# Kernel tuning notes

Measured on AMD Instinct MI355X. Metric: run time of the kernel, lower is better.

Reference implementation:

```python
import math
import jax, jax.numpy as jnp
import numpy as np

C1, D, NUM_HEADS, K_CH = 150, 32, 4, 10
GLOBAL_TOPK_RATIO = 0.08


def _pos2d(h, w, dim):
    d2 = dim // 2
    div = jnp.exp(jnp.arange(0, d2, 2, dtype=jnp.float32) * (-(math.log(10000.0) / d2)))
    def axis_pe(n):
        ang = jnp.arange(n, dtype=jnp.float32)[:, None] * div[None, :]
        pe = jnp.zeros((n, d2), dtype=jnp.float32)
        pe = pe.at[:, 0::2].set(jnp.sin(ang))
        pe = pe.at[:, 1::2].set(jnp.cos(ang))
        return pe
    pe_y = axis_pe(h)  # [h, d2]
    pe_x = axis_pe(w)  # [w, d2]
    return jnp.concatenate([
        jnp.broadcast_to(pe_y[:, None, :], (h, w, d2)),
        jnp.broadcast_to(pe_x[None, :, :], (h, w, d2)),
    ], axis=-1)  # [h, w, dim]


def setup_inputs() -> dict:
    key = jax.random.key(0)
    ks = jax.random.split(key, 7)
    B = 1024
    return {
        "x": jax.random.uniform(ks[0], (B, 1, 28, 28), dtype=jnp.float32),
        "conv1_w": jax.random.normal(ks[1], (C1, 1, 9, 9), dtype=jnp.float32) * 0.05,
        "channel_embed": jax.random.normal(ks[2], (C1, D), dtype=jnp.float32) * 0.02,
        "in_proj_w": jax.random.normal(ks[3], (3 * D, D), dtype=jnp.float32) * (1.0 / math.sqrt(D)),
        "in_proj_b": jnp.zeros((3 * D,), dtype=jnp.float32),
        "out_proj_w": jax.random.normal(ks[4], (D, D), dtype=jnp.float32) * (1.0 / math.sqrt(D)),
        "out_proj_b": jnp.zeros((D,), dtype=jnp.float32),
    }


def reference(x, conv1_w, channel_embed, in_proj_w, in_proj_b, out_proj_w, out_proj_b):
    # conv1 + relu: [B,1,28,28] -> [B,150,14,14]
    A = jax.nn.relu(jax.lax.conv_general_dilated(
        x, conv1_w, window_strides=(2, 2), padding=((4, 4), (4, 4)),
        dimension_numbers=("NCHW", "OIHW", "NCHW")))
    B, C, H, W = A.shape
    total = C * H * W
    k_global = max(1, int(math.ceil(GLOBAL_TOPK_RATIO * total)))
    A_flat = A.reshape(B, -1)
    # global kthvalue threshold: k_global-th largest per sample
    thresh = jax.lax.top_k(A_flat, k_global)[0][:, -1:]
    A_global = (A_flat * (A_flat >= thresh)).reshape(B, C, H, W)
    # per-location channel top-k + scatter
    v = jnp.transpose(A_global, (0, 2, 3, 1))  # [B,H,W,C]
    topv, topi = jax.lax.top_k(v, K_CH)        # [B,H,W,k]
    N = B * H * W
    logits = jnp.zeros((N, C), v.dtype).at[
        jnp.arange(N)[:, None], topi.reshape(N, K_CH)
    ].set(topv.reshape(N, K_CH)).reshape(v.shape)
    # normalize by per-sample global max (guard zero)
    flat_logits = logits.reshape(B, -1)
    gmax = jnp.max(flat_logits, axis=1, keepdims=True)
    normed = jnp.where(gmax == 0, 0.0, flat_logits / jnp.where(gmax == 0, 1.0, gmax))
    sparse_weights = normed.reshape(logits.shape)  # [B,H,W,C]
    # channel embedding + 2D sinusoidal PE
    loc_emb = jnp.einsum("bhwc,cd->bhwd", sparse_weights, channel_embed)
    loc_emb = loc_emb + _pos2d(H, W, D)[None]
    seq = loc_emb.reshape(B, H * W, D)
    # 1-layer MHA (self-attention, batch_first)
    qkv = seq @ in_proj_w.T + in_proj_b  # [B,S,3D]
    q, k, vv = jnp.split(qkv, 3, axis=-1)
    hd = D // NUM_HEADS
    def heads(t):
        return jnp.transpose(t.reshape(B, H * W, NUM_HEADS, hd), (0, 2, 1, 3))
    q, k, vv = heads(q), heads(k), heads(vv)
    attn = jax.nn.softmax(jnp.einsum("bnsd,bntd->bnst", q, k) / math.sqrt(hd), axis=-1)
    ctx = jnp.einsum("bnst,bntd->bnsd", attn, vv)
    ctx = jnp.transpose(ctx, (0, 2, 1, 3)).reshape(B, H * W, D)
    attn_out = ctx @ out_proj_w.T + out_proj_b  # [B, 196, 32]
    return attn_out
```

## Files before the change

kernel.cpp:

```cpp
#include <hip/hip_runtime.h>
#include <math.h>

#define NC1 150
#define HW 196
#define NB 1024
#define DD 32
#define NHD 4
#define HDIM 8
#define KG 2352
#define KCH 10
#define CAP 48
#define CVS 49
#define CES 36
#define KVS 20

typedef float v2f __attribute__((ext_vector_type(2)));

__device__ __forceinline__ float dot32v(const v2f* __restrict__ xr2,
                                        const float* __restrict__ wr, float bias) {
  const float4* w4 = (const float4*)wr;
  v2f s0 = {bias, 0.f};
  v2f s1 = {0.f, 0.f};
#pragma unroll
  for (int e = 0; e < 8; ++e) {
    float4 w = w4[e];
    v2f wlo = {w.x, w.y}, whi = {w.z, w.w};
    s0 = __builtin_elementwise_fma(xr2[2 * e], wlo, s0);
    s1 = __builtin_elementwise_fma(xr2[2 * e + 1], whi, s1);
  }
  v2f s = s0 + s1;
  return s.x + s.y;
}

#define UNI_F 17552
#define XT_OFF 0
#define WT_OFF 8232
#define CV_OFF 0
#define CC_OFF 9604
#define CNT_OFF 11956
#define CE_OFF 12152

__global__ void prep2_kernel(const float* __restrict__ cw, float* __restrict__ wtg,
                             float* __restrict__ pos) {
  int i = blockIdx.x * 256 + threadIdx.x;
  if (i < HW * DD) {
    int s = i >> 5, d = i & 31;
    int h = s / 14, w = s % 14;
    int p = (d < 16) ? h : w;
    int dd = (d < 16) ? d : d - 16;
    int j = dd >> 1;
    float dv = expf(-(logf(10000.0f) / 16.0f) * (float)(2 * j));
    float ang = (float)p * dv;
    pos[i] = (dd & 1) ? cosf(ang) : sinf(ang);
    return;
  }
  int j = i - HW * DD;
  if (j < 84 * 152) {
    int k = j / 152, c = j - k * 152;
    wtg[j] = (k < 81 && c < NC1) ? cw[c * 81 + k] : 0.f;
  }
}

__global__ __launch_bounds__(1024, 8) void fused_kernel(const float* __restrict__ x,
                                                        const float* __restrict__ wtg,
                                                        const float* __restrict__ CE,
                                                        const float* __restrict__ pos,
                                                        float* __restrict__ seqo) {
  __shared__ alignas(16) float uni[UNI_F];
  __shared__ alignas(16) float xs[784];
  __shared__ unsigned hist[2048];
  __shared__ unsigned wsum[4];
  __shared__ unsigned s_prefix, s_krem, s_max;

  int b = blockIdx.x, tid = threadIdx.x;
  int lane = tid & 63, wid = tid >> 6;

  if (tid < 196) ((float4*)xs)[tid] = ((const float4*)(x + (size_t)b * 784))[tid];
  if (tid == 0) { s_prefix = 0u; s_krem = KG; s_max = 0u; }
  __syncthreads();

  int cg = tid / 49;
  int g  = tid - cg * 49;
  bool act = (tid < 931);
  float acc[4][8];
#pragma unroll
  for (int i = 0; i < 4; ++i)
#pragma unroll
    for (int j = 0; j < 8; ++j) acc[i][j] = 0.f;

  float* XT = uni + XT_OFF;
  float* WT = uni + WT_OFF;

  for (int kb = 0; kb < 84; kb += 42) {
    for (int i = tid; i < 42 * 196; i += 1024) {
      int kk = i / 196, s = i - kk * 196;
      int k = kb + kk;
      float v = 0.f;
      if (k < 81) {
        int ki = k / 9, kj = k - ki * 9;
        int h = s / 14, w = s - h * 14;
        int r = 2 * h - 4 + ki, c = 2 * w - 4 + kj;
        if (r >= 0 && r < 28 && c >= 0 && c < 28) v = xs[r * 28 + c];
      }
      XT[i] = v;
    }
    for (int i = tid; i < (42 * 152) / 4; i += 1024)
      ((float4*)WT)[i] = ((const float4*)(wtg + kb * 152))[i];
    __syncthreads();
    if (act) {
      const float* xtp = XT + 4 * g;
      const float* wtp = WT + 8 * cg;
#pragma unroll 7
      for (int kk = 0; kk < 42; ++kk) {
        float4 xv = *(const float4*)(xtp + kk * 196);
        float4 w0 = *(const float4*)(wtp + kk * 152);
        float4 w1 = *(const float4*)(wtp + kk * 152 + 4);
        float xa[4] = {xv.x, xv.y, xv.z, xv.w};
        float wa[8] = {w0.x, w0.y, w0.z, w0.w, w1.x, w1.y, w1.z, w1.w};
#pragma unroll
        for (int i = 0; i < 4; ++i)
#pragma unroll
          for (int j = 0; j < 8; ++j) acc[i][j] += xa[i] * wa[j];
      }
    }
    __syncthreads();
  }

#pragma unroll
  for (int i = 0; i < 4; ++i)
#pragma unroll
    for (int j = 0; j < 8; ++j) acc[i][j] = fmaxf(acc[i][j], 0.f);

  for (int pass = 0; pass < 3; ++pass) {
    hist[tid] = 0u; hist[tid + 1024] = 0u;
    __syncthreads();
    int shift = (pass == 0) ? 21 : (pass == 1 ? 10 : 0);
    int bits = (pass == 2) ? 10 : 11;
    unsigned mask = (1u << bits) - 1u;
    unsigned pfx = s_prefix;
    unsigned krem = s_krem;
    int hishift = shift + bits;
    if (pass == 0) {
      unsigned mymax = 0u;
#pragma unroll
      for (int i = 0; i < 4; ++i)
#pragma unroll
        for (int j = 0; j < 8; ++j) {
          unsigned u = __float_as_uint(acc[i][j]);
          mymax = max(mymax, u);
          if (u) atomicAdd(&hist[u >> 21], 1u);
        }
#pragma unroll
      for (int st = 32; st >= 1; st >>= 1)
        mymax = max(mymax, (unsigned)__shfl_xor((int)mymax, st));
      if (lane == 0) atomicMax(&s_max, mymax);
    } else {
#pragma unroll
      for (int i = 0; i < 4; ++i)
#pragma unroll
        for (int j = 0; j < 8; ++j) {
          unsigned u = __float_as_uint(acc[i][j]);
          if (u && (u >> hishift) == pfx) atomicAdd(&hist[(u >> shift) & mask], 1u);
        }
    }
    __syncthreads();
    int segsz = (1 << bits) >> 8;
    unsigned segv = 0u, sufv = 0u;
    if (tid < 256) {
      for (int j = 0; j < segsz; ++j) segv += hist[tid * segsz + j];
      sufv = segv;
#pragma unroll
      for (int st = 1; st < 64; st <<= 1) {
        unsigned o = (unsigned)__shfl_down((int)sufv, st);
        if (lane + st < 64) sufv += o;
      }
      if (lane == 0) wsum[wid] = sufv;
    }
    __syncthreads();
    if (tid < 256) {
      unsigned tail = 0u;
      for (int ww = wid + 1; ww < 4; ++ww) tail += wsum[ww];
      sufv += tail;
      unsigned above = sufv - segv;
      if (above < krem && sufv >= krem) {
        unsigned cum = above;
        int dsel = tid * segsz;
        for (int d2 = segsz - 1; d2 >= 0; --d2) {
          int dd = tid * segsz + d2;
          if (cum + hist[dd] >= krem) { dsel = dd; break; }
          cum += hist[dd];
        }
        s_prefix = (pfx << bits) | (unsigned)dsel;
        s_krem = krem - cum;
      }
    }
    __syncthreads();
  }

  float* candV = uni + CV_OFF;
  unsigned char* candC = (unsigned char*)(uni + CC_OFF);
  unsigned* cnt = (unsigned*)(uni + CNT_OFF);
  if (tid < 196) cnt[tid] = 0u;
  __syncthreads();
  float T = __uint_as_float(s_prefix);
  if (act) {
#pragma unroll
    for (int i = 0; i < 4; ++i) {
      int loc = 4 * g + i;
#pragma unroll
      for (int j = 0; j < 8; ++j) {
        float v = acc[i][j];
        if (v >= T && v > 0.f) {
          unsigned slot = atomicAdd(&cnt[loc], 1u);
          if (slot < CAP) {
            candV[loc * CVS + slot] = v;
            candC[loc * CAP + slot] = (unsigned char)(8 * cg + j);
          }
        }
      }
    }
  }
  __syncthreads();

  float* CEs = uni + CE_OFF;
  if (tid >= 196) {
    for (int i = tid - 196; i < NC1 * 32; i += 1024 - 196) {
      int c = i >> 5, e = i & 31;
      CEs[c * CES + e] = CE[i];
    }
  }
  float tv[KCH]; int tc[KCH];
  if (tid < 196) {
    int loc = tid;
    unsigned n = cnt[loc]; if (n > CAP) n = CAP;
#pragma unroll
    for (int k = 0; k < KCH; ++k) { tv[k] = 0.f; tc[k] = 0; }
    for (unsigned jj = 0; jj < n; ++jj) {
      float v = candV[loc * CVS + jj];
      int c = candC[loc * CAP + jj];
      if (v > tv[KCH - 1] || (v == tv[KCH - 1] && c < tc[KCH - 1])) {
        float iv = v; int ic = c;
#pragma unroll
        for (int j = 0; j < KCH; ++j) {
          bool gt = (iv > tv[j]) || (iv == tv[j] && ic < tc[j]);
          float nv = gt ? iv : tv[j]; int nc = gt ? ic : tc[j];
          float ov = gt ? tv[j] : iv; int oc = gt ? tc[j] : ic;
          tv[j] = nv; tc[j] = nc; iv = ov; ic = oc;
        }
      }
    }
  }
  __syncthreads();

  if (tid < 196) {
    float gm = __uint_as_float(s_max);
    float gi = (gm == 0.0f) ? 0.0f : 1.0f / gm;
    float acc2[32];
#pragma unroll
    for (int e = 0; e < 32; ++e) acc2[e] = 0.f;
#pragma unroll
    for (int k = 0; k < KCH; ++k) {
      float v = tv[k];
      const float4* cr = (const float4*)(CEs + tc[k] * CES);
#pragma unroll
      for (int e4 = 0; e4 < 8; ++e4) {
        float4 cv = cr[e4];
        acc2[e4 * 4 + 0] += v * cv.x;
        acc2[e4 * 4 + 1] += v * cv.y;
        acc2[e4 * 4 + 2] += v * cv.z;
        acc2[e4 * 4 + 3] += v * cv.w;
      }
    }
    float* op = seqo + ((size_t)b * HW + tid) * DD;
    const float* pr = pos + tid * DD;
#pragma unroll
    for (int e4 = 0; e4 < 8; ++e4) {
      float4 pv = ((const float4*)pr)[e4];
      float4 o;
      o.x = acc2[e4 * 4 + 0] * gi + pv.x;
      o.y = acc2[e4 * 4 + 1] * gi + pv.y;
      o.z = acc2[e4 * 4 + 2] * gi + pv.z;
      o.w = acc2[e4 * 4 + 3] * gi + pv.w;
      ((float4*)op)[e4] = o;
    }
  }
}

__global__ __launch_bounds__(832, 3) void attn_kernel(const float* __restrict__ seq,
                                                      const float* __restrict__ Wqkv,
                                                      const float* __restrict__ bqkv,
                                                      float* __restrict__ ctxo) {
  __shared__ alignas(16) float kvs[NHD * HW * KVS];
  __shared__ alignas(16) float swq[96 * DD];
  __shared__ float sbq[96];
  __shared__ unsigned s_kk[NHD];

  int b = blockIdx.x, tid = threadIdx.x;
  int h = tid / HW;
  int s = tid - h * HW;
  bool act = (tid < NHD * HW);

  v2f xr2[16];
  if (act) {
    const float4* row4 = (const float4*)(seq + ((size_t)b * HW + s) * DD);
#pragma unroll
    for (int e = 0; e < 8; ++e) {
      float4 f = row4[e];
      v2f lo = {f.x, f.y}, hi = {f.z, f.w};
      xr2[2 * e] = lo; xr2[2 * e + 1] = hi;
    }
  }
  for (int i = tid; i < (96 * DD) / 4; i += 832)
    ((float4*)swq)[i] = ((const float4*)Wqkv)[i];
  if (tid < 96) sbq[tid] = bqkv[tid];
  if (tid < NHD) s_kk[tid] = 0u;
  __syncthreads();

  v2f q01, q23, q45, q67;
  float qq = 0.f;
  if (act) {
    float* kvrow = kvs + (h * HW + s) * KVS;
    {
      float ka[8]; float kk = 0.f;
#pragma unroll
      for (int d = 0; d < 8; ++d) {
        ka[d] = dot32v(xr2, swq + (32 + h * HDIM + d) * DD, sbq[32 + h * HDIM + d]);
        kk += ka[d] * ka[d];
      }
      float4 k0 = {ka[0], ka[1], ka[2], ka[3]}, k1 = {ka[4], ka[5], ka[6], ka[7]};
      ((float4*)kvrow)[0] = k0; ((float4*)kvrow)[1] = k1;
      atomicMax(&s_kk[h], __float_as_uint(kk));
    }
    {
      float va[8];
#pragma unroll
      for (int d = 0; d < 8; ++d)
        va[d] = dot32v(xr2, swq + (64 + h * HDIM + d) * DD, sbq[64 + h * HDIM + d]);
      float4 v0 = {va[0], va[1], va[2], va[3]}, v1 = {va[4], va[5], va[6], va[7]};
      ((float4*)kvrow)[2] = v0; ((float4*)kvrow)[3] = v1;
    }
    float qa[8];
#pragma unroll
    for (int d = 0; d < 8; ++d) {
      qa[d] = dot32v(xr2, swq + (h * HDIM + d) * DD, sbq[h * HDIM + d]);
      qq += qa[d] * qa[d];
    }
    q01.x = qa[0]; q01.y = qa[1]; q23.x = qa[2]; q23.y = qa[3];
    q45.x = qa[4]; q45.y = qa[5]; q67.x = qa[6]; q67.y = qa[7];
  }
  __syncthreads();
  if (!act) return;

  const float scaleL = 0.3535533905932738f * 1.4426950408889634f;
  float kkmax = __uint_as_float(s_kk[h]);
  float negML = -sqrtf(qq * kkmax) * scaleL;
  float l = 0.f;
  v2f c01 = {0.f, 0.f}, c23 = {0.f, 0.f}, c45 = {0.f, 0.f}, c67 = {0.f, 0.f};
  const float4* kp = (const float4*)(kvs + (h * HW) * KVS);
#pragma unroll 4
  for (int t = 0; t < HW; ++t) {
    float4 k0 = kp[0], k1 = kp[1], v0 = kp[2], v1 = kp[3];
    kp += 5;
    v2f k0lo = {k0.x, k0.y}, k0hi = {k0.z, k0.w};
    v2f k1lo = {k1.x, k1.y}, k1hi = {k1.z, k1.w};
    v2f d = q01 * k0lo;
    d = __builtin_elementwise_fma(q23, k0hi, d);
    d = __builtin_elementwise_fma(q45, k1lo, d);
    d = __builtin_elementwise_fma(q67, k1hi, d);
    float sc = d.x + d.y;
    float p = exp2f(fmaf(sc, scaleL, negML));
    l += p;
    v2f pp = {p, p};
    v2f v0lo = {v0.x, v0.y}, v0hi = {v0.z, v0.w};
    v2f v1lo = {v1.x, v1.y}, v1hi = {v1.z, v1.w};
    c01 = __builtin_elementwise_fma(pp, v0lo, c01);
    c23 = __builtin_elementwise_fma(pp, v0hi, c23);
    c45 = __builtin_elementwise_fma(pp, v1lo, c45);
    c67 = __builtin_elementwise_fma(pp, v1hi, c67);
  }
  float inv = 1.0f / l;
  float* op = ctxo + ((size_t)b * HW + s) * DD + h * HDIM;
  float4 o0, o1;
  o0.x = c01.x * inv; o0.y = c01.y * inv; o0.z = c23.x * inv; o0.w = c23.y * inv;
  o1.x = c45.x * inv; o1.y = c45.y * inv; o1.z = c67.x * inv; o1.w = c67.y * inv;
  ((float4*)op)[0] = o0; ((float4*)op)[1] = o1;
}

__global__ __launch_bounds__(256) void outproj_kernel(const float* __restrict__ ctx,
                                                      const float* __restrict__ Wo,
                                                      const float* __restrict__ bo,
                                                      float* __restrict__ out) {
  __shared__ float sw[32 * 32];
  __shared__ float sb2[32];
  int tid = threadIdx.x;
  for (int i = tid; i < 1024; i += 256) sw[i] = Wo[i];
  if (tid < 32) sb2[tid] = bo[tid];
  __syncthreads();
  size_t row = (size_t)blockIdx.x * 256 + tid;
  const float* cr = ctx + row * 32;
  v2f xr2[16];
#pragma unroll
  for (int e = 0; e < 8; ++e) {
    float4 f = ((const float4*)cr)[e];
    v2f lo = {f.x, f.y}, hi = {f.z, f.w};
    xr2[2 * e] = lo; xr2[2 * e + 1] = hi;
  }
  float* op = out + row * 32;
#pragma unroll
  for (int d4 = 0; d4 < 8; ++d4) {
    float4 o;
    float* oo = (float*)&o;
#pragma unroll
    for (int q = 0; q < 4; ++q) {
      int d = d4 * 4 + q;
      oo[q] = dot32v(xr2, sw + d * 32, sb2[d]);
    }
    ((float4*)op)[d4] = o;
  }
}

extern "C" void kernel_launch(void* const* d_in, const int* in_sizes, int n_in,
                              void* d_out, int out_size, void* d_ws, size_t ws_size,
                              hipStream_t stream) {
  const float* x  = (const float*)d_in[0];
  const float* cw = (const float*)d_in[1];
  const float* ce = (const float*)d_in[2];
  const float* wq = (const float*)d_in[3];
  const float* bq = (const float*)d_in[4];
  const float* wo = (const float*)d_in[5];
  const float* bo = (const float*)d_in[6];
  float* out = (float*)d_out;
  float* ws  = (float*)d_ws;

  float* ctx = ws;
  float* pos = ws + (size_t)NB * HW * DD;
  float* wtg = pos + HW * DD;

  prep2_kernel<<<(HW * DD + 84 * 152 + 255) / 256, 256, 0, stream>>>(cw, wtg, pos);
  fused_kernel<<<NB, 1024, 0, stream>>>(x, wtg, ce, pos, out);
  attn_kernel<<<NB, 832, 0, stream>>>(out, wq, bq, ctx);
  outproj_kernel<<<(NB * HW * DD) / (256 * 32), 256, 0, stream>>>(ctx, wo, bo, out);
}
```

Measured before the change: 384.3 us.

## Process two queries per thread in attention loop to reuse K/V loads

Q vectors are now staged in shared memory, and after the projection phase only 392 threads stay active. Each of them handles two query rows of the same head, so every K/V row read from LDS serves two queries. This halves LDS traffic per score and adds ILP. The cost is more registers per thread, half the threads idle in the attention loop (fewer waves to hide latency), and extra shared memory for the Q staging, which may reduce blocks per CU.

```diff
diff --git a/kernel.cpp b/kernel.cpp
--- a/kernel.cpp
+++ b/kernel.cpp
@@ -13,6 +13,7 @@
 #define CVS 49
 #define CES 36
 #define KVS 20
+#define QLS 12
 
 typedef float v2f __attribute__((ext_vector_type(2)));
 
@@ -291,6 +292,7 @@
                                                       const float* __restrict__ bqkv,
                                                       float* __restrict__ ctxo) {
   __shared__ alignas(16) float kvs[NHD * HW * KVS];
+  __shared__ alignas(16) float qls[NHD * HW * QLS];
   __shared__ alignas(16) float swq[96 * DD];
   __shared__ float sbq[96];
   __shared__ unsigned s_kk[NHD];
@@ -316,8 +318,6 @@
   if (tid < NHD) s_kk[tid] = 0u;
   __syncthreads();
 
-  v2f q01, q23, q45, q67;
-  float qq = 0.f;
   if (act) {
     float* kvrow = kvs + (h * HW + s) * KVS;
     {
@@ -339,51 +339,87 @@
       float4 v0 = {va[0], va[1], va[2], va[3]}, v1 = {va[4], va[5], va[6], va[7]};
       ((float4*)kvrow)[2] = v0; ((float4*)kvrow)[3] = v1;
     }
-    float qa[8];
-#pragma unroll
-    for (int d = 0; d < 8; ++d) {
-      qa[d] = dot32v(xr2, swq + (h * HDIM + d) * DD, sbq[h * HDIM + d]);
-      qq += qa[d] * qa[d];
-    }
-    q01.x = qa[0]; q01.y = qa[1]; q23.x = qa[2]; q23.y = qa[3];
-    q45.x = qa[4]; q45.y = qa[5]; q67.x = qa[6]; q67.y = qa[7];
-  }
-  __syncthreads();
-  if (!act) return;
-
+    {
+      float qa8[8];
+#pragma unroll
+      for (int d = 0; d < 8; ++d)
+        qa8[d] = dot32v(xr2, swq + (h * HDIM + d) * DD, sbq[h * HDIM + d]);
+      float* qrow = qls + (h * HW + s) * QLS;
+      float4 q0 = {qa8[0], qa8[1], qa8[2], qa8[3]}, q1 = {qa8[4], qa8[5], qa8[6], qa8[7]};
+      ((float4*)qrow)[0] = q0; ((float4*)qrow)[1] = q1;
+    }
+  }
+  __syncthreads();
+  if (tid >= 392) return;
+
+  int h2 = tid / 98, s0 = tid - h2 * 98;
+  v2f qa[4], qb[4];
+  {
+    const float4* qra = (const float4*)(qls + (h2 * HW + s0) * QLS);
+    const float4* qrb = (const float4*)(qls + (h2 * HW + s0 + 98) * QLS);
+    float4 a0 = qra[0], a1 = qra[1], b0 = qrb[0], b1 = qrb[1];
+    qa[0].x = a0.x; qa[0].y = a0.y; qa[1].x = a0.z; qa[1].y = a0.w;
+    qa[2].x = a1.x; qa[2].y = a1.y; qa[3].x = a1.z; qa[3].y = a1.w;
+    qb[0].x = b0.x; qb[0].y = b0.y; qb[1].x = b0.z; qb[1].y = b0.w;
+    qb[2].x = b1.x; qb[2].y = b1.y; qb[3].x = b1.z; qb[3].y = b1.w;
+  }
   const float scaleL = 0.3535533905932738f * 1.4426950408889634f;
-  float kkmax = __uint_as_float(s_kk[h]);
-  float negML = -sqrtf(qq * kkmax) * scaleL;
-  float l = 0.f;
-  v2f c01 = {0.f, 0.f}, c23 = {0.f, 0.f}, c45 = {0.f, 0.f}, c67 = {0.f, 0.f};
-  const float4* kp = (const float4*)(kvs + (h * HW) * KVS);
-#pragma unroll 4
+  float kkmax = __uint_as_float(s_kk[h2]);
+  v2f t2;
+  t2 = qa[0] * qa[0];
+  t2 = __builtin_elementwise_fma(qa[1], qa[1], t2);
+  t2 = __builtin_elementwise_fma(qa[2], qa[2], t2);
+  t2 = __builtin_elementwise_fma(qa[3], qa[3], t2);
+  float negMLa = -sqrtf((t2.x + t2.y) * kkmax) * scaleL;
+  t2 = qb[0] * qb[0];
+  t2 = __builtin_elementwise_fma(qb[1], qb[1], t2);
+  t2 = __builtin_elementwise_fma(qb[2], qb[2], t2);
+  t2 = __builtin_elementwise_fma(qb[3], qb[3], t2);
+  float negMLb = -sqrtf((t2.x + t2.y) * kkmax) * scaleL;
+
+  float la = 0.f, lb = 0.f;
+  v2f ca01 = {0.f, 0.f}, ca23 = {0.f, 0.f}, ca45 = {0.f, 0.f}, ca67 = {0.f, 0.f};
+  v2f cb01 = {0.f, 0.f}, cb23 = {0.f, 0.f}, cb45 = {0.f, 0.f}, cb67 = {0.f, 0.f};
+  const float4* kp = (const float4*)(kvs + (h2 * HW) * KVS);
+#pragma unroll 2
   for (int t = 0; t < HW; ++t) {
     float4 k0 = kp[0], k1 = kp[1], v0 = kp[2], v1 = kp[3];
     kp += 5;
     v2f k0lo = {k0.x, k0.y}, k0hi = {k0.z, k0.w};
     v2f k1lo = {k1.x, k1.y}, k1hi = {k1.z, k1.w};
-    v2f d = q01 * k0lo;
-    d = __builtin_elementwise_fma(q23, k0hi, d);
-    d = __builtin_elementwise_fma(q45, k1lo, d);
-    d = __builtin_elementwise_fma(q67, k1hi, d);
-    float sc = d.x + d.y;
-    float p = exp2f(fmaf(sc, scaleL, negML));
-    l += p;
-    v2f pp = {p, p};
+    v2f da = qa[0] * k0lo;
+    da = __builtin_elementwise_fma(qa[1], k0hi, da);
+    da = __builtin_elementwise_fma(qa[2], k1lo, da);
+    da = __builtin_elementwise_fma(qa[3], k1hi, da);
+    v2f db = qb[0] * k0lo;
+    db = __builtin_elementwise_fma(qb[1], k0hi, db);
+    db = __builtin_elementwise_fma(qb[2], k1lo, db);
+    db = __builtin_elementwise_fma(qb[3], k1hi, db);
+    float pa = exp2f(fmaf(da.x + da.y, scaleL, negMLa));
+    float pb = exp2f(fmaf(db.x + db.y, scaleL, negMLb));
+    la += pa; lb += pb;
+    v2f ppa = {pa, pa}, ppb = {pb, pb};
     v2f v0lo = {v0.x, v0.y}, v0hi = {v0.z, v0.w};
     v2f v1lo = {v1.x, v1.y}, v1hi = {v1.z, v1.w};
-    c01 = __builtin_elementwise_fma(pp, v0lo, c01);
-    c23 = __builtin_elementwise_fma(pp, v0hi, c23);
-    c45 = __builtin_elementwise_fma(pp, v1lo, c45);
-    c67 = __builtin_elementwise_fma(pp, v1hi, c67);
-  }
-  float inv = 1.0f / l;
-  float* op = ctxo + ((size_t)b * HW + s) * DD + h * HDIM;
+    ca01 = __builtin_elementwise_fma(ppa, v0lo, ca01);
+    ca23 = __builtin_elementwise_fma(ppa, v0hi, ca23);
+    ca45 = __builtin_elementwise_fma(ppa, v1lo, ca45);
+    ca67 = __builtin_elementwise_fma(ppa, v1hi, ca67);
+    cb01 = __builtin_elementwise_fma(ppb, v0lo, cb01);
+    cb23 = __builtin_elementwise_fma(ppb, v0hi, cb23);
+    cb45 = __builtin_elementwise_fma(ppb, v1lo, cb45);
+    cb67 = __builtin_elementwise_fma(ppb, v1hi, cb67);
+  }
+  float inva = 1.0f / la, invb = 1.0f / lb;
+  float* opa = ctxo + ((size_t)b * HW + s0) * DD + h2 * HDIM;
+  float* opb = ctxo + ((size_t)b * HW + s0 + 98) * DD + h2 * HDIM;
   float4 o0, o1;
-  o0.x = c01.x * inv; o0.y = c01.y * inv; o0.z = c23.x * inv; o0.w = c23.y * inv;
-  o1.x = c45.x * inv; o1.y = c45.y * inv; o1.z = c67.x * inv; o1.w = c67.y * inv;
-  ((float4*)op)[0] = o0; ((float4*)op)[1] = o1;
+  o0.x = ca01.x * inva; o0.y = ca01.y * inva; o0.z = ca23.x * inva; o0.w = ca23.y * inva;
+  o1.x = ca45.x * inva; o1.y = ca45.y * inva; o1.z = ca67.x * inva; o1.w = ca67.y * inva;
+  ((float4*)opa)[0] = o0; ((float4*)opa)[1] = o1;
+  o0.x = cb01.x * invb; o0.y = cb01.y * invb; o0.z = cb23.x * invb; o0.w = cb23.y * invb;
+  o1.x = cb45.x * invb; o1.y = cb45.y * invb; o1.z = cb67.x * invb; o1.w = cb67.y * invb;
+  ((float4*)opb)[0] = o0; ((float4*)opb)[1] = o1;
 }
 
 __global__ __launch_bounds__(256) void outproj_kernel(const float* __restrict__ ctx,
```

Measured after the change: 404.5 us. 1.05x slower.
